# Performance work log

Measured on AMD Instinct MI355X. Metric: run time of the kernel, lower is better.

Reference implementation:

```python
import math
import jax, jax.numpy as jnp
import numpy as np
from jax import lax

B, S, ENC_IN = 8, 1024, 3
D_MODEL, N_HEADS, D_FF, E_LAYERS = 512, 8, 2048, 3
FACTOR, NUM_CLASS = 5, 5
EPS = 1e-5


def _positional_embedding(seq_len, d_model):
    pos = np.arange(seq_len)[:, None].astype(np.float32)
    div = np.exp(np.arange(0, d_model, 2).astype(np.float32) * -(math.log(10000.0) / d_model))
    pe = np.zeros((seq_len, d_model), dtype=np.float32)
    pe[:, 0::2] = np.sin(pos * div)
    pe[:, 1::2] = np.cos(pos * div)
    return jnp.asarray(pe)


def _layer_norm(x, g, b):
    mu = x.mean(-1, keepdims=True)
    var = ((x - mu) ** 2).mean(-1, keepdims=True)
    return (x - mu) / jnp.sqrt(var + EPS) * g + b


def _prob_attention(Q, K, V, key):
    # Q, K, V: (B, H, L, Dh). Informer ProbSparse self-attention (mask_flag=False).
    Bq, H, L, Dh = Q.shape
    sample_k = min(FACTOR * math.ceil(math.log(L)), L)  # U_part
    n_top = min(FACTOR * math.ceil(math.log(L)), L)     # u
    idx = jax.random.randint(key, (L, sample_k), 0, L)  # sampled key idx per query
    K_sample = K[:, :, idx, :]                          # (B,H,L,sample_k,Dh)
    QK_sample = jnp.einsum('bhld,bhlsd->bhls', Q, K_sample)
    M = QK_sample.max(-1) - QK_sample.sum(-1) / L       # sparsity measure (B,H,L)
    M_top = lax.top_k(M, n_top)[1]                      # (B,H,n_top)
    Q_reduce = jnp.take_along_axis(Q, M_top[..., None], axis=2)  # (B,H,n_top,Dh)
    scores = jnp.einsum('bhud,bhkd->bhuk', Q_reduce, K) / math.sqrt(Dh)
    attn = jax.nn.softmax(scores, axis=-1)
    upd = jnp.einsum('bhuk,bhkd->bhud', attn, V)        # (B,H,n_top,Dh)
    # initial context = mean of V over keys; active queries get real attention
    context = jnp.broadcast_to(V.mean(axis=2, keepdims=True), Q.shape)
    b_idx = jnp.arange(Bq)[:, None, None]
    h_idx = jnp.arange(H)[None, :, None]
    return context.at[b_idx, h_idx, M_top].set(upd)     # (B,H,L,Dh)


def _encoder_layer(x, p, key):
    (wq, bq, wk, bk, wv, bv, wo, bo, c1w, c1b, c2w, c2b, g1, b1, g2, b2) = p
    Bx, L, D = x.shape
    Dh = D // N_HEADS

    def heads(w, b_):
        return (x @ w.T + b_).reshape(Bx, L, N_HEADS, Dh).transpose(0, 2, 1, 3)

    Q, K, V = heads(wq, bq), heads(wk, bk), heads(wv, bv)
    ctx = _prob_attention(Q, K, V, key)
    new_x = ctx.transpose(0, 2, 1, 3).reshape(Bx, L, D) @ wo.T + bo
    x = _layer_norm(x + new_x, g1, b1)
    y = jax.nn.gelu(x @ c1w.T + c1b, approximate=False)  # 1x1 conv == matmul
    y = y @ c2w.T + c2b
    return _layer_norm(x + y, g2, b2)


def _forward(x_enc, x_mark_enc, token_kernel, Wq, bq, Wk, bk, Wv, bv, Wo, bo,
             c1w, c1b, c2w, c2b, g1, b1, g2, b2, gf, bf, proj_w, proj_b):
    # TokenEmbedding: circular Conv1d(enc_in -> d_model, kernel 3), no bias
    xp = jnp.concatenate([x_enc[:, -1:], x_enc, x_enc[:, :1]], axis=1)
    val = lax.conv_general_dilated(xp, token_kernel, (1,), 'VALID',
                                   dimension_numbers=('NWC', 'WIO', 'NWC'))
    x = val + _positional_embedding(S, D_MODEL)[None]  # dropout = 0 (eval)
    base = jax.random.key(42)
    for i in range(E_LAYERS):
        p = (Wq[i], bq[i], Wk[i], bk[i], Wv[i], bv[i], Wo[i], bo[i],
             c1w[i], c1b[i], c2w[i], c2b[i], g1[i], b1[i], g2[i], b2[i])
        x = _encoder_layer(x, p, jax.random.fold_in(base, i))
    x = _layer_norm(x, gf, bf)
    out = jax.nn.gelu(x, approximate=False)
    out = out * x_mark_enc[..., None]
    out = out.reshape(out.shape[0], -1)
    return out @ proj_w.T + proj_b  # (B, NUM_CLASS)


def setup_inputs():
    key = jax.random.key(0)
    ks = jax.random.split(key, 16)
    s = 0.02
    L, D, F = E_LAYERS, D_MODEL, D_FF

    def rn(k, shape, scale=s):
        return jax.random.normal(k, shape, jnp.float32) * scale

    return {
        'x_enc': jax.random.normal(ks[0], (B, S, ENC_IN), jnp.float32),
        'x_mark_enc': jnp.ones((B, S), jnp.float32),
        'token_kernel': rn(ks[1], (3, ENC_IN, D)),
        'Wq': rn(ks[2], (L, D, D)), 'bq': jnp.zeros((L, D), jnp.float32),
        'Wk': rn(ks[3], (L, D, D)), 'bk': jnp.zeros((L, D), jnp.float32),
        'Wv': rn(ks[4], (L, D, D)), 'bv': jnp.zeros((L, D), jnp.float32),
        'Wo': rn(ks[5], (L, D, D)), 'bo': jnp.zeros((L, D), jnp.float32),
        'c1w': rn(ks[6], (L, F, D)), 'c1b': jnp.zeros((L, F), jnp.float32),
        'c2w': rn(ks[7], (L, D, F)), 'c2b': jnp.zeros((L, D), jnp.float32),
        'g1': jnp.ones((L, D), jnp.float32), 'b1': jnp.zeros((L, D), jnp.float32),
        'g2': jnp.ones((L, D), jnp.float32), 'b2': jnp.zeros((L, D), jnp.float32),
        'gf': jnp.ones((D,), jnp.float32), 'bf': jnp.zeros((D,), jnp.float32),
        'proj_w': rn(ks[8], (NUM_CLASS, D * S), 0.002),
        'proj_b': jnp.zeros((NUM_CLASS,), jnp.float32),
    }


def reference(x_enc, x_mark_enc, token_kernel, Wq, bq, Wk, bk, Wv, bv, Wo, bo,
              c1w, c1b, c2w, c2b, g1, b1, g2, b2, gf, bf, proj_w, proj_b):
    return _forward(x_enc, x_mark_enc, token_kernel, Wq, bq, Wk, bk, Wv, bv, Wo, bo,
                    c1w, c1b, c2w, c2b, g1, b1, g2, b2, gf, bf, proj_w, proj_b)
```

## Files before the change

### kernel.cpp

```cpp
#include <hip/hip_runtime.h>
#include <hip/hip_bf16.h>
#include <stdint.h>


#define SQ 1024
#define DM 512
#define NH 8
#define DH 64
#define DFF 2048
#define NTOP 35
#define ROWS 8192
#define QKVD 1536
#define EPSF 1e-5f
#define KSPLIT 8
#define SSPLIT 4

typedef __attribute__((ext_vector_type(8))) short bf16x8;
typedef __attribute__((ext_vector_type(4))) float f32x4;

__device__ __forceinline__ void gload_lds16(const void* g, void* l) {
    __builtin_amdgcn_global_load_lds((const __attribute__((address_space(1))) void*)g,
                                     (__attribute__((address_space(3))) void*)l, 16, 0, 0);
}

__device__ inline float gelu_f(float v) {
    return 0.5f * v * (1.0f + erff(v * 0.7071067811865476f));
}

__device__ __forceinline__ void split_hl(float v, __hip_bfloat16& h, __hip_bfloat16& l) {
    h = __float2bfloat16(v);
    l = __float2bfloat16(v - __bfloat162float(h));
}

__device__ inline void tf_round(uint32_t& x0, uint32_t& x1, int r) {
    x0 += x1;
    x1 = (x1 << r) | (x1 >> (32 - r));
    x1 ^= x0;
}
__device__ inline uint2 tf2x32(uint32_t k0, uint32_t k1, uint32_t x0, uint32_t x1) {
    uint32_t ks2 = k0 ^ k1 ^ 0x1BD11BDAu;
    x0 += k0; x1 += k1;
    tf_round(x0,x1,13); tf_round(x0,x1,15); tf_round(x0,x1,26); tf_round(x0,x1,6);
    x0 += k1; x1 += ks2 + 1u;
    tf_round(x0,x1,17); tf_round(x0,x1,29); tf_round(x0,x1,16); tf_round(x0,x1,24);
    x0 += ks2; x1 += k0 + 2u;
    tf_round(x0,x1,13); tf_round(x0,x1,15); tf_round(x0,x1,26); tf_round(x0,x1,6);
    x0 += k0; x1 += k1 + 3u;
    tf_round(x0,x1,17); tf_round(x0,x1,29); tf_round(x0,x1,16); tf_round(x0,x1,24);
    x0 += k1; x1 += ks2 + 4u;
    tf_round(x0,x1,13); tf_round(x0,x1,15); tf_round(x0,x1,26); tf_round(x0,x1,6);
    x0 += ks2; x1 += k0 + 5u;
    return make_uint2(x0, x1);
}

__global__ void idx_kernel(int lyr, int* __restrict__ idx) {
    int p = blockIdx.x * 256 + threadIdx.x;
    if (p >= SQ * NTOP) return;
    uint2 fk = tf2x32(0u, 42u, 0u, (uint32_t)lyr);
    uint2 a = tf2x32(fk.x, fk.y, 0u, 2u);
    uint2 bb = tf2x32(fk.x, fk.y, 1u, 3u);
    uint32_t k20 = a.y, k21 = bb.y;
    const int half = (SQ * NTOP) / 2;
    uint32_t bits;
    if (p < half) bits = tf2x32(k20, k21, (uint32_t)p, (uint32_t)(half + p)).x;
    else          bits = tf2x32(k20, k21, (uint32_t)(p - half), (uint32_t)p).y;
    idx[p] = (int)(bits & 1023u);
}

__global__ __launch_bounds__(256) void embed_kernel(const float* __restrict__ xe,
                                                    const float* __restrict__ tk,
                                                    float* __restrict__ X,
                                                    __hip_bfloat16* __restrict__ Xh,
                                                    __hip_bfloat16* __restrict__ Xl) {
    int row = blockIdx.x;
    int b = row >> 10, s = row & 1023;
    __shared__ float xv[9];
    int t = threadIdx.x;
    if (t < 9) {
        int w = t / 3, c = t % 3;
        int tt = s + w;
        int r = (tt == 0) ? 1023 : (tt <= 1024 ? tt - 1 : 0);
        xv[t] = xe[((size_t)b * SQ + r) * 3 + c];
    }
    __syncthreads();
    const float cdiv = 0.017988946039015984f;
    for (int d = t; d < DM; d += 256) {
        float acc = 0.f;
        #pragma unroll
        for (int wi = 0; wi < 9; ++wi) acc += xv[wi] * tk[wi * DM + d];
        int j2 = (d >> 1) * 2;
        float div = expf(-cdiv * (float)j2);
        float ang = (float)s * div;
        float pe = (d & 1) ? cosf(ang) : sinf(ang);
        float v = acc + pe;
        size_t o = (size_t)row * DM + d;
        X[o] = v;
        __hip_bfloat16 hb, lb; split_hl(v, hb, lb);
        Xh[o] = hb; Xl[o] = lb;
    }
}

__global__ __launch_bounds__(256) void wsplitA_kernel(
    const float* __restrict__ Wq, const float* __restrict__ Wk,
    const float* __restrict__ Wv, const float* __restrict__ Wo,
    const float* __restrict__ bq, const float* __restrict__ bk,
    const float* __restrict__ bv,
    __hip_bfloat16* __restrict__ ha, __hip_bfloat16* __restrict__ la,
    __hip_bfloat16* __restrict__ hb, __hip_bfloat16* __restrict__ lb,
    float* __restrict__ biasC) {
    int t = threadIdx.x;
    if (blockIdx.x == 1024) {
        #pragma unroll
        for (int r = 0; r < 6; ++r) {
            int i = r * 256 + t;
            biasC[i] = (i < 512) ? bq[i] : (i < 1024) ? bk[i - 512] : bv[i - 1024];
        }
        return;
    }
    int i = blockIdx.x * 256 + t;
    int seg = i >> 16, local = i & 65535;
    const float* srcs[4] = {Wq, Wk, Wv, Wo};
    float4 v = reinterpret_cast<const float4*>(srcs[seg])[local];
    float vv[4] = {v.x, v.y, v.z, v.w};
    ushort hv[4], lv[4];
    #pragma unroll
    for (int j = 0; j < 4; ++j) {
        __hip_bfloat16 h_, l_; split_hl(vv[j], h_, l_);
        hv[j] = *reinterpret_cast<ushort*>(&h_);
        lv[j] = *reinterpret_cast<ushort*>(&l_);
    }
    ushort4 hq = make_ushort4(hv[0], hv[1], hv[2], hv[3]);
    ushort4 lq = make_ushort4(lv[0], lv[1], lv[2], lv[3]);
    if (seg < 3) {
        reinterpret_cast<ushort4*>(ha)[i] = hq;
        reinterpret_cast<ushort4*>(la)[i] = lq;
    } else {
        reinterpret_cast<ushort4*>(hb)[local] = hq;
        reinterpret_cast<ushort4*>(lb)[local] = lq;
    }
}

__global__ __launch_bounds__(256) void wsplitB_kernel(
    const float* __restrict__ c1w, const float* __restrict__ c2w,
    __hip_bfloat16* __restrict__ ha, __hip_bfloat16* __restrict__ la,
    __hip_bfloat16* __restrict__ hb, __hip_bfloat16* __restrict__ lb) {
    int i = blockIdx.x * 256 + threadIdx.x;
    int seg = i >> 18, local = i & 262143;
    const float* src = seg ? c2w : c1w;
    float4 v = reinterpret_cast<const float4*>(src)[local];
    float vv[4] = {v.x, v.y, v.z, v.w};
    ushort hv[4], lv[4];
    #pragma unroll
    for (int j = 0; j < 4; ++j) {
        __hip_bfloat16 h_, l_; split_hl(vv[j], h_, l_);
        hv[j] = *reinterpret_cast<ushort*>(&h_);
        lv[j] = *reinterpret_cast<ushort*>(&l_);
    }
    ushort4 hq = make_ushort4(hv[0], hv[1], hv[2], hv[3]);
    ushort4 lq = make_ushort4(lv[0], lv[1], lv[2], lv[3]);
    if (seg == 0) {
        reinterpret_cast<ushort4*>(ha)[local] = hq;
        reinterpret_cast<ushort4*>(la)[local] = lq;
    } else {
        reinterpret_cast<ushort4*>(hb)[local] = hq;
        reinterpret_cast<ushort4*>(lb)[local] = lq;
    }
}

template<int BN_, int OUTMODE, int NTERM>
__global__ __launch_bounds__(256) void mfma_gemm(
    const __hip_bfloat16* __restrict__ Ah, const __hip_bfloat16* __restrict__ Al,
    const __hip_bfloat16* __restrict__ Wh, const __hip_bfloat16* __restrict__ Wl,
    const float* __restrict__ bias,
    float* __restrict__ C,
    __hip_bfloat16* __restrict__ Oh, __hip_bfloat16* __restrict__ Ol,
    int M, int N, int K) {
    constexpr int NI = BN_ / 32;
    __shared__ __hip_bfloat16 As[128 * 64];
    __shared__ __hip_bfloat16 Bs[BN_ * 64];
    const int t = threadIdx.x;
    const int lane = t & 63, w = t >> 6;
    const int wm = w >> 1, wn = w & 1;
    const int bm = blockIdx.x * 128, bn = blockIdx.y * BN_;
    const int r15 = lane & 15, kc = lane >> 4;
    f32x4 acc[4][NI];
    #pragma unroll
    for (int mi = 0; mi < 4; ++mi)
        #pragma unroll
        for (int ni = 0; ni < NI; ++ni)
            acc[mi][ni] = (f32x4){0.f, 0.f, 0.f, 0.f};

    const int KT = NTERM * K;
    for (int kp = 0; kp < KT; kp += 64) {
        int seg = (NTERM == 3) ? ((kp >= 2 * K) ? 2 : ((kp >= K) ? 1 : 0))
                               : ((kp >= K) ? 1 : 0);
        int k0 = kp - seg * K;
        const __hip_bfloat16* Ab = (seg == 1) ? Al : Ah;
        const __hip_bfloat16* Bb = (NTERM == 3 && seg == 2) ? Wl : Wh;
        #pragma unroll
        for (int i = 0; i < 4; ++i) {
            int slot = i * 256 + t;
            int row = slot >> 3, cp = slot & 7;
            int cl = cp ^ (row & 7);
            gload_lds16(Ab + (size_t)(bm + row) * K + k0 + cl * 8, As + slot * 8);
        }
        #pragma unroll
        for (int i = 0; i < BN_ / 32; ++i) {
            int slot = i * 256 + t;
            int row = slot >> 3, cp = slot & 7;
            int cl = cp ^ (row & 7);
            gload_lds16(Bb + (size_t)(bn + row) * K + k0 + cl * 8, Bs + slot * 8);
        }
        __syncthreads();
        #pragma unroll
        for (int kk = 0; kk < 2; ++kk) {
            bf16x8 a[4], b[NI];
            #pragma unroll
            for (int mi = 0; mi < 4; ++mi) {
                int row = wm * 64 + mi * 16 + r15;
                int sl = ((kk << 2) | kc) ^ (row & 7);
                a[mi] = *reinterpret_cast<const bf16x8*>(As + row * 64 + sl * 8);
            }
            #pragma unroll
            for (int ni = 0; ni < NI; ++ni) {
                int row = wn * (BN_ / 2) + ni * 16 + r15;
                int sl = ((kk << 2) | kc) ^ (row & 7);
                b[ni] = *reinterpret_cast<const bf16x8*>(Bs + row * 64 + sl * 8);
            }
            #pragma unroll
            for (int mi = 0; mi < 4; ++mi)
                #pragma unroll
                for (int ni = 0; ni < NI; ++ni)
                    acc[mi][ni] = __builtin_amdgcn_mfma_f32_16x16x32_bf16(a[mi], b[ni], acc[mi][ni], 0, 0, 0);
        }
        __syncthreads();
    }

    const int rq = lane >> 4;
    #pragma unroll
    for (int mi = 0; mi < 4; ++mi) {
        #pragma unroll
        for (int ni = 0; ni < NI; ++ni) {
            int n = bn + wn * (BN_ / 2) + ni * 16 + r15;
            float bz = bias[n];
            #pragma unroll
            for (int r = 0; r < 4; ++r) {
                int m = bm + wm * 64 + mi * 16 + rq * 4 + r;
                float v = acc[mi][ni][r] + bz;
                if constexpr (OUTMODE == 0) {
                    C[(size_t)m * N + n] = v;
                } else {
                    float g = gelu_f(v);
                    __hip_bfloat16 hb, lb; split_hl(g, hb, lb);
                    Oh[(size_t)m * N + n] = hb;
                    Ol[(size_t)m * N + n] = lb;
                }
            }
        }
    }
}

__global__ __launch_bounds__(128) void mscore_part(const float* __restrict__ QKV,
                                                   const int* __restrict__ idx,
                                                   float* __restrict__ MX,
                                                   float* __restrict__ SM) {
    int bh = blockIdx.x;
    int l = blockIdx.y * 128 + threadIdx.x;
    int sc = blockIdx.z;
    int b = bh >> 3, h = bh & 7;
    const float4* q = reinterpret_cast<const float4*>(QKV + ((size_t)(b * SQ + l)) * QKVD + h * DH);
    float4 qr[16];
    #pragma unroll
    for (int i = 0; i < 16; ++i) qr[i] = q[i];
    int s0 = sc * 9;
    int s1 = (s0 + 9 < NTOP) ? s0 + 9 : NTOP;
    float mx = -INFINITY, sm = 0.f;
    for (int s = s0; s < s1; ++s) {
        int ki = idx[l * NTOP + s];
        const float4* kr = reinterpret_cast<const float4*>(QKV + ((size_t)(b * SQ + ki)) * QKVD + DM + h * DH);
        float d = 0.f;
        #pragma unroll
        for (int i = 0; i < 16; ++i) {
            float4 kv = kr[i];
            d += qr[i].x * kv.x + qr[i].y * kv.y + qr[i].z * kv.z + qr[i].w * kv.w;
        }
        mx = fmaxf(mx, d);
        sm += d;
    }
    size_t o = ((size_t)(bh * SSPLIT + sc) << 10) + l;
    MX[o] = mx; SM[o] = sm;
}

__global__ __launch_bounds__(256) void topk_kernel(const float* __restrict__ MX,
                                                   const float* __restrict__ SM,
                                                   int* __restrict__ Mtop) {
    int bh = blockIdx.x;
    int t = threadIdx.x, w = t >> 6, lane = t & 63;
    float v[4];
    #pragma unroll
    for (int j = 0; j < 4; ++j) {
        int i = j * 256 + t;
        float mx = -INFINITY, sm = 0.f;
        #pragma unroll
        for (int sc = 0; sc < SSPLIT; ++sc) {
            size_t o = ((size_t)(bh * SSPLIT + sc) << 10) + i;
            mx = fmaxf(mx, MX[o]);
            sm += SM[o];
        }
        v[j] = mx - sm * (1.0f / (float)SQ);
    }
    __shared__ float swv[4];
    __shared__ int swi[4];
    __shared__ int winner;
    for (int u = 0; u < NTOP; ++u) {
        float bv = v[0]; int bj = 0;
        #pragma unroll
        for (int j = 1; j < 4; ++j)
            if (v[j] > bv) { bv = v[j]; bj = j; }
        int bi = bj * 256 + t;
        #pragma unroll
        for (int off = 32; off; off >>= 1) {
            float ov = __shfl_xor(bv, off);
            int oi = __shfl_xor(bi, off);
            if (ov > bv || (ov == bv && oi < bi)) { bv = ov; bi = oi; }
        }
        if (lane == 0) { swv[w] = bv; swi[w] = bi; }
        __syncthreads();
        if (t == 0) {
            float gv = swv[0]; int gi = swi[0];
            #pragma unroll
            for (int k = 1; k < 4; ++k)
                if (swv[k] > gv || (swv[k] == gv && swi[k] < gi)) { gv = swv[k]; gi = swi[k]; }
            Mtop[bh * NTOP + u] = gi;
            winner = gi;
        }
        __syncthreads();
        int wi = winner;
        if ((wi & 255) == t) v[wi >> 8] = -INFINITY;
    }
}

__global__ __launch_bounds__(512) void attn_part(const float* __restrict__ QKV,
                                                 const int* __restrict__ Mtop,
                                                 float* __restrict__ PACC,
                                                 float* __restrict__ PM,
                                                 float* __restrict__ PL) {
    __shared__ float Qs[NTOP][68];
    __shared__ float Kt[64][68];
    __shared__ float Vt[64][68];
    __shared__ float St[NTOP][64];
    __shared__ float mS[NTOP], lS[NTOP], fS[NTOP];
    __shared__ int qidx[NTOP];
    int bh = blockIdx.x, ks = blockIdx.y;
    int b = bh >> 3, h = bh & 7;
    int t = threadIdx.x, w = t >> 6, lane = t & 63;
    if (t < NTOP) { qidx[t] = Mtop[bh * NTOP + t]; mS[t] = -INFINITY; lS[t] = 0.f; }
    __syncthreads();
    for (int u = w; u < NTOP; u += 8)
        Qs[u][lane] = QKV[((size_t)(b * SQ + qidx[u])) * QKVD + h * DH + lane];
    float a_acc[5] = {0.f, 0.f, 0.f, 0.f, 0.f};
    __syncthreads();
    for (int tk = ks * 2; tk < ks * 2 + 2; ++tk) {
        #pragma unroll
        for (int i = 0; i < 2; ++i) {
            int idx4 = i * 512 + t;
            int kr = idx4 >> 4, c4 = (idx4 & 15) << 2;
            const float* kp = QKV + ((size_t)(b * SQ + tk * 64 + kr)) * QKVD + DM + h * DH + c4;
            *reinterpret_cast<float4*>(&Kt[kr][c4]) = *reinterpret_cast<const float4*>(kp);
            *reinterpret_cast<float4*>(&Vt[kr][c4]) = *reinterpret_cast<const float4*>(kp + DM);
        }
        __syncthreads();
        float sv[5] = {0.f, 0.f, 0.f, 0.f, 0.f};
        #pragma unroll
        for (int d4 = 0; d4 < 16; ++d4) {
            float4 kv = *reinterpret_cast<const float4*>(&Kt[lane][d4 << 2]);
            #pragma unroll
            for (int j = 0; j < 5; ++j) {
                int u = w + 8 * j;
                if (u < NTOP) {
                    float4 qv = *reinterpret_cast<const float4*>(&Qs[u][d4 << 2]);
                    sv[j] += qv.x * kv.x + qv.y * kv.y + qv.z * kv.z + qv.w * kv.w;
                }
            }
        }
        #pragma unroll
        for (int j = 0; j < 5; ++j) {
            int u = w + 8 * j;
            if (u < NTOP) {
                float s = sv[j] * 0.125f;
                float mx = s;
                #pragma unroll
                for (int off = 32; off; off >>= 1) mx = fmaxf(mx, __shfl_xor(mx, off));
                float m_old = mS[u];
                float m_new = fmaxf(m_old, mx);
                float e = expf(s - m_new);
                float sum = e;
                #pragma unroll
                for (int off = 32; off; off >>= 1) sum += __shfl_xor(sum, off);
                St[u][lane] = e;
                if (lane == 0) {
                    float f = expf(m_old - m_new);
                    fS[u] = f;
                    lS[u] = lS[u] * f + sum;
                    mS[u] = m_new;
                }
            }
        }
        __syncthreads();
        #pragma unroll
        for (int j = 0; j < 5; ++j) {
            int u = w + 8 * j;
            if (u < NTOP) {
                float acc = a_acc[j] * fS[u];
                for (int k = 0; k < 64; ++k)
                    acc += St[u][k] * Vt[k][lane];
                a_acc[j] = acc;
            }
        }
        __syncthreads();
    }
    #pragma unroll
    for (int j = 0; j < 5; ++j) {
        int u = w + 8 * j;
        if (u < NTOP) {
            PACC[(((size_t)bh * KSPLIT + ks) * NTOP + u) * DH + lane] = a_acc[j];
            if (lane == 0) {
                PM[((size_t)bh * KSPLIT + ks) * NTOP + u] = mS[u];
                PL[((size_t)bh * KSPLIT + ks) * NTOP + u] = lS[u];
            }
        }
    }
}

__global__ __launch_bounds__(512) void attn_comb(const float* __restrict__ PACC,
                                                 const float* __restrict__ PM,
                                                 const float* __restrict__ PL,
                                                 const int* __restrict__ Mtop,
                                                 __hip_bfloat16* __restrict__ ch,
                                                 __hip_bfloat16* __restrict__ cl) {
    int bh = blockIdx.x;
    int b = bh >> 3, h = bh & 7;
    int t = threadIdx.x, w = t >> 6, lane = t & 63;
    #pragma unroll
    for (int j = 0; j < 5; ++j) {
        int u = w + 8 * j;
        if (u < NTOP) {
            float M = -INFINITY;
            #pragma unroll
            for (int i = 0; i < KSPLIT; ++i)
                M = fmaxf(M, PM[((size_t)bh * KSPLIT + i) * NTOP + u]);
            float lsum = 0.f, acc = 0.f;
            #pragma unroll
            for (int i = 0; i < KSPLIT; ++i) {
                float f = expf(PM[((size_t)bh * KSPLIT + i) * NTOP + u] - M);
                lsum += f * PL[((size_t)bh * KSPLIT + i) * NTOP + u];
                acc += f * PACC[(((size_t)bh * KSPLIT + i) * NTOP + u) * DH + lane];
            }
            float v = acc / lsum;
            int l = Mtop[bh * NTOP + u];
            size_t o = ((size_t)(b * SQ + l)) * DM + h * DH + lane;
            __hip_bfloat16 hb, lb; split_hl(v, hb, lb);
            ch[o] = hb; cl[o] = lb;
        }
    }
}

__global__ __launch_bounds__(256) void meanv_part(const float* __restrict__ QKV,
                                                  float* __restrict__ part) {
    int bh = blockIdx.x, sp = blockIdx.y;
    int t = threadIdx.x;
    int b = bh >> 3, h = bh & 7;
    int dh = t & 63, chunk = t >> 6;
    int s0 = sp * 128 + chunk * 32;
    float acc = 0.f;
    for (int s = s0; s < s0 + 32; ++s)
        acc += QKV[((size_t)(b * SQ + s)) * QKVD + 2 * DM + h * DH + dh];
    __shared__ float red[256];
    red[t] = acc; __syncthreads();
    if (t < 64)
        part[((size_t)bh * 8 + sp) * DH + dh] =
            red[t] + red[64 + t] + red[128 + t] + red[192 + t];
}

__global__ void meanv_comb(const float* __restrict__ part, float* __restrict__ meanV) {
    int bh = blockIdx.x;
    int t = threadIdx.x;
    float s = 0.f;
    #pragma unroll
    for (int i = 0; i < 8; ++i) s += part[((size_t)bh * 8 + i) * DH + t];
    meanV[bh * DH + t] = s * (1.0f / (float)SQ);
}

__global__ void ctxfill2_kernel(const float* __restrict__ meanV,
                                __hip_bfloat16* __restrict__ ch,
                                __hip_bfloat16* __restrict__ cl) {
    int n = blockIdx.x * 256 + threadIdx.x;
    int d = n & 511;
    int row = n >> 9;
    int b = row >> 10;
    float v = meanV[((b << 3) + (d >> 6)) * DH + (d & 63)];
    __hip_bfloat16 hb, lb; split_hl(v, hb, lb);
    ch[n] = hb; cl[n] = lb;
}

__global__ __launch_bounds__(256) void add_ln_kernel(const float* __restrict__ Av,
                                                     const float* __restrict__ Bv,
                                                     const float* __restrict__ g,
                                                     const float* __restrict__ be,
                                                     float* __restrict__ out,
                                                     __hip_bfloat16* __restrict__ oh,
                                                     __hip_bfloat16* __restrict__ ol) {
    int row = blockIdx.x;
    int t = threadIdx.x;
    size_t base = (size_t)row * DM;
    float v0 = Av[base + t] + Bv[base + t];
    float v1 = Av[base + 256 + t] + Bv[base + 256 + t];
    __shared__ float r1[256], r2[256];
    r1[t] = v0 + v1; r2[t] = v0 * v0 + v1 * v1;
    __syncthreads();
    for (int s = 128; s > 0; s >>= 1) {
        if (t < s) { r1[t] += r1[t + s]; r2[t] += r2[t + s]; }
        __syncthreads();
    }
    float mu = r1[0] * (1.0f / (float)DM);
    float var = r2[0] * (1.0f / (float)DM) - mu * mu;
    float rs = rsqrtf(var + EPSF);
    float o0 = (v0 - mu) * rs * g[t] + be[t];
    float o1 = (v1 - mu) * rs * g[t + 256] + be[t + 256];
    out[base + t] = o0;
    out[base + 256 + t] = o1;
    __hip_bfloat16 hb, lb;
    split_hl(o0, hb, lb); oh[base + t] = hb; ol[base + t] = lb;
    split_hl(o1, hb, lb); oh[base + 256 + t] = hb; ol[base + 256 + t] = lb;
}

__global__ __launch_bounds__(256) void final_kernel(const float* __restrict__ X,
                                                    const float* __restrict__ g,
                                                    const float* __restrict__ be,
                                                    const float* __restrict__ mark,
                                                    float* __restrict__ act) {
    int row = blockIdx.x;
    int t = threadIdx.x;
    size_t base = (size_t)row * DM;
    float v0 = X[base + t];
    float v1 = X[base + 256 + t];
    __shared__ float r1[256], r2[256];
    r1[t] = v0 + v1; r2[t] = v0 * v0 + v1 * v1;
    __syncthreads();
    for (int s = 128; s > 0; s >>= 1) {
        if (t < s) { r1[t] += r1[t + s]; r2[t] += r2[t + s]; }
        __syncthreads();
    }
    float mu = r1[0] * (1.0f / (float)DM);
    float var = r2[0] * (1.0f / (float)DM) - mu * mu;
    float rs = rsqrtf(var + EPSF);
    float mk = mark[row];
    float a0 = (v0 - mu) * rs * g[t] + be[t];
    float a1 = (v1 - mu) * rs * g[t + 256] + be[t + 256];
    act[base + t] = gelu_f(a0) * mk;
    act[base + 256 + t] = gelu_f(a1) * mk;
}

__global__ __launch_bounds__(256) void proj1_kernel(const float* __restrict__ act,
                                                    const float* __restrict__ pw,
                                                    float* __restrict__ part) {
    int bc = blockIdx.x;
    int sg = blockIdx.y;
    int b = bc / 5, c = bc % 5;
    const float4* a = reinterpret_cast<const float4*>(act + (size_t)b * (SQ * DM) + sg * 32768);
    const float4* w = reinterpret_cast<const float4*>(pw + (size_t)c * (SQ * DM) + sg * 32768);
    float s = 0.f;
    for (int i = threadIdx.x; i < 8192; i += 256) {
        float4 av = a[i], wv = w[i];
        s += av.x * wv.x + av.y * wv.y + av.z * wv.z + av.w * wv.w;
    }
    __shared__ float red[256];
    red[threadIdx.x] = s; __syncthreads();
    for (int sft = 128; sft > 0; sft >>= 1) {
        if (threadIdx.x < sft) red[threadIdx.x] += red[threadIdx.x + sft];
        __syncthreads();
    }
    if (threadIdx.x == 0) part[bc * 16 + sg] = red[0];
}

__global__ void proj2_kernel(const float* __restrict__ part, const float* __restrict__ pb,
                             float* __restrict__ out) {
    int t = threadIdx.x;
    if (t < 40) {
        float s = 0.f;
        #pragma unroll
        for (int i = 0; i < 16; ++i) s += part[t * 16 + i];
        out[t] = s + pb[t % 5];
    }
}

extern "C" void kernel_launch(void* const* d_in, const int* in_sizes, int n_in,
                              void* d_out, int out_size, void* d_ws, size_t ws_size,
                              hipStream_t stream) {
    (void)in_sizes; (void)n_in; (void)out_size; (void)ws_size;

    const float* x_enc      = (const float*)d_in[0];
    const float* x_mark_enc = (const float*)d_in[1];
    const float* token_k    = (const float*)d_in[2];
    const float* Wq = (const float*)d_in[3];
    const float* bq = (const float*)d_in[4];
    const float* Wk = (const float*)d_in[5];
    const float* bk = (const float*)d_in[6];
    const float* Wv = (const float*)d_in[7];
    const float* bv = (const float*)d_in[8];
    const float* Wo = (const float*)d_in[9];
    const float* bo = (const float*)d_in[10];
    const float* c1w = (const float*)d_in[11];
    const float* c1b = (const float*)d_in[12];
    const float* c2w = (const float*)d_in[13];
    const float* c2b = (const float*)d_in[14];
    const float* g1 = (const float*)d_in[15];
    const float* b1 = (const float*)d_in[16];
    const float* g2 = (const float*)d_in[17];
    const float* b2 = (const float*)d_in[18];
    const float* gf = (const float*)d_in[19];
    const float* bf = (const float*)d_in[20];
    const float* proj_w = (const float*)d_in[21];
    const float* proj_b = (const float*)d_in[22];
    float* out = (float*)d_out;

    const size_t MB = 1024 * 1024;
    char* wsb = (char*)d_ws;
    float* X    = (float*)(wsb);
    float* QKVp = (float*)(wsb + 16 * MB);
    __hip_bfloat16* CTXh = (__hip_bfloat16*)(wsb + 16 * MB);
    __hip_bfloat16* CTXl = (__hip_bfloat16*)(wsb + 24 * MB);
    __hip_bfloat16* Yh   = (__hip_bfloat16*)(wsb);
    __hip_bfloat16* Yl   = (__hip_bfloat16*)(wsb + 32 * MB);
    float* X1p  = (float*)(wsb + 64 * MB);
    float* NXp  = (float*)(wsb + 80 * MB);
    __hip_bfloat16* Xh  = (__hip_bfloat16*)(wsb + 96 * MB);
    __hip_bfloat16* Xl  = (__hip_bfloat16*)(wsb + 104 * MB);
    __hip_bfloat16* X1h = (__hip_bfloat16*)(wsb + 112 * MB);
    __hip_bfloat16* X1l = (__hip_bfloat16*)(wsb + 120 * MB);
    __hip_bfloat16* WhA = (__hip_bfloat16*)(wsb + 128 * MB);
    __hip_bfloat16* WlA = (__hip_bfloat16*)(wsb + 130 * MB);
    __hip_bfloat16* WhB = (__hip_bfloat16*)(wsb + 132 * MB);
    __hip_bfloat16* WlB = (__hip_bfloat16*)(wsb + 134 * MB);
    char* smal = wsb + 136 * MB;
    float* biasC  = (float*)(smal);
    int*   IDX    = (int*)(smal + 8 * 1024);
    int*   MTOP   = (int*)(smal + 168 * 1024);
    float* MEANV  = (float*)(smal + 184 * 1024);
    float* PART   = (float*)(smal + 200 * 1024);
    float* MVPART = (float*)(smal + 208 * 1024);
    float* MX     = (float*)(smal + 384 * 1024);
    float* SM     = (float*)(smal + 2176 * 1024);
    float* PM     = (float*)(smal + 3968 * 1024);
    float* PL     = (float*)(smal + 4064 * 1024);
    float* PACC   = (float*)(smal + 4160 * 1024);

    embed_kernel<<<ROWS, 256, 0, stream>>>(x_enc, token_k, X, Xh, Xl);

    for (int lyr = 0; lyr < 3; ++lyr) {
        const float* Wq_l = Wq + (size_t)lyr * DM * DM;
        const float* bq_l = bq + (size_t)lyr * DM;
        const float* Wk_l = Wk + (size_t)lyr * DM * DM;
        const float* bk_l = bk + (size_t)lyr * DM;
        const float* Wv_l = Wv + (size_t)lyr * DM * DM;
        const float* bv_l = bv + (size_t)lyr * DM;
        const float* Wo_l = Wo + (size_t)lyr * DM * DM;
        const float* bo_l = bo + (size_t)lyr * DM;
        const float* c1w_l = c1w + (size_t)lyr * DFF * DM;
        const float* c1b_l = c1b + (size_t)lyr * DFF;
        const float* c2w_l = c2w + (size_t)lyr * DM * DFF;
        const float* c2b_l = c2b + (size_t)lyr * DM;
        const float* g1_l = g1 + (size_t)lyr * DM;
        const float* b1_l = b1 + (size_t)lyr * DM;
        const float* g2_l = g2 + (size_t)lyr * DM;
        const float* b2_l = b2 + (size_t)lyr * DM;

        wsplitA_kernel<<<1025, 256, 0, stream>>>(Wq_l, Wk_l, Wv_l, Wo_l,
                                                 bq_l, bk_l, bv_l,
                                                 WhA, WlA, WhB, WlB, biasC);
        mfma_gemm<128, 0, 3><<<dim3(ROWS / 128, QKVD / 128), 256, 0, stream>>>(
            Xh, Xl, WhA, WlA, biasC, QKVp, nullptr, nullptr, ROWS, QKVD, DM);

        idx_kernel<<<(SQ * NTOP + 255) / 256, 256, 0, stream>>>(lyr, IDX);
        mscore_part<<<dim3(64, 8, SSPLIT), 128, 0, stream>>>(QKVp, IDX, MX, SM);
        topk_kernel<<<64, 256, 0, stream>>>(MX, SM, MTOP);
        attn_part<<<dim3(64, KSPLIT), 512, 0, stream>>>(QKVp, MTOP, PACC, PM, PL);
        meanv_part<<<dim3(64, 8), 256, 0, stream>>>(QKVp, MVPART);
        meanv_comb<<<64, 64, 0, stream>>>(MVPART, MEANV);
        ctxfill2_kernel<<<(ROWS * DM) / 256, 256, 0, stream>>>(MEANV, CTXh, CTXl);
        attn_comb<<<64, 512, 0, stream>>>(PACC, PM, PL, MTOP, CTXh, CTXl);

        mfma_gemm<64, 0, 2><<<dim3(ROWS / 128, DM / 64), 256, 0, stream>>>(
            CTXh, CTXl, WhB, WlB, bo_l, NXp, nullptr, nullptr, ROWS, DM, DM);
        add_ln_kernel<<<ROWS, 256, 0, stream>>>(X, NXp, g1_l, b1_l, X1p, X1h, X1l);

        wsplitB_kernel<<<2048, 256, 0, stream>>>(c1w_l, c2w_l, WhA, WlA, WhB, WlB);
        mfma_gemm<128, 2, 2><<<dim3(ROWS / 128, DFF / 128), 256, 0, stream>>>(
            X1h, X1l, WhA, WlA, c1b_l, nullptr, Yh, Yl, ROWS, DFF, DM);
        mfma_gemm<64, 0, 2><<<dim3(ROWS / 128, DM / 64), 256, 0, stream>>>(
            Yh, Yl, WhB, WlB, c2b_l, NXp, nullptr, nullptr, ROWS, DM, DFF);
        add_ln_kernel<<<ROWS, 256, 0, stream>>>(X1p, NXp, g2_l, b2_l, X, Xh, Xl);
    }

    final_kernel<<<ROWS, 256, 0, stream>>>(X, gf, bf, x_mark_enc, (float*)QKVp);
    proj1_kernel<<<dim3(40, 16), 256, 0, stream>>>((float*)QKVp, proj_w, PART);
    proj2_kernel<<<1, 64, 0, stream>>>(PART, proj_b, out);
}
```

Before: 1.373 ms.

## Compute sparsity scores with 16 lanes per query and shuffle reduction

The sparsity-measure kernel now assigns each query row to 16 lanes, each holding one float4 of Q. Each sampled K row is read as a coalesced 256-byte access and the dot product is reduced with xor shuffles. This replaces one thread per query reading a full K row, which produced scattered per-thread loads, plus the 4-way split across sample chunks. The split partials are gone, so topk reads the final max and sum directly. The cost is four shuffle rounds per sampled key and more threads in total.

```diff
diff --git a/kernel.cpp b/kernel.cpp
--- a/kernel.cpp
+++ b/kernel.cpp
@@ -13,7 +13,6 @@
 #define QKVD 1536
 #define EPSF 1e-5f
 #define KSPLIT 8
-#define SSPLIT 4
 
 typedef __attribute__((ext_vector_type(8))) short bf16x8;
 typedef __attribute__((ext_vector_type(4))) float f32x4;
@@ -260,35 +259,36 @@
     }
 }
 
-__global__ __launch_bounds__(128) void mscore_part(const float* __restrict__ QKV,
+__global__ __launch_bounds__(512) void mscore_wave(const float* __restrict__ QKV,
                                                    const int* __restrict__ idx,
                                                    float* __restrict__ MX,
                                                    float* __restrict__ SM) {
     int bh = blockIdx.x;
-    int l = blockIdx.y * 128 + threadIdx.x;
-    int sc = blockIdx.z;
     int b = bh >> 3, h = bh & 7;
-    const float4* q = reinterpret_cast<const float4*>(QKV + ((size_t)(b * SQ + l)) * QKVD + h * DH);
-    float4 qr[16];
-    #pragma unroll
-    for (int i = 0; i < 16; ++i) qr[i] = q[i];
-    int s0 = sc * 9;
-    int s1 = (s0 + 9 < NTOP) ? s0 + 9 : NTOP;
+    int t = threadIdx.x;
+    int wv = t >> 6, lane = t & 63;
+    int r = lane >> 4;
+    int d4 = lane & 15;
+    int l = blockIdx.y * 32 + wv * 4 + r;
+    const float* qbase = QKV + ((size_t)(b * SQ + l)) * QKVD + h * DH;
+    float4 q = reinterpret_cast<const float4*>(qbase)[d4];
+    const float* Kbase = QKV + (size_t)b * SQ * QKVD + DM + h * DH;
+    const int* ib = idx + l * NTOP;
     float mx = -INFINITY, sm = 0.f;
-    for (int s = s0; s < s1; ++s) {
-        int ki = idx[l * NTOP + s];
-        const float4* kr = reinterpret_cast<const float4*>(QKV + ((size_t)(b * SQ + ki)) * QKVD + DM + h * DH);
-        float d = 0.f;
-        #pragma unroll
-        for (int i = 0; i < 16; ++i) {
-            float4 kv = kr[i];
-            d += qr[i].x * kv.x + qr[i].y * kv.y + qr[i].z * kv.z + qr[i].w * kv.w;
-        }
+    #pragma unroll 7
+    for (int s = 0; s < NTOP; ++s) {
+        int ki = ib[s];
+        float4 kv = reinterpret_cast<const float4*>(Kbase + (size_t)ki * QKVD)[d4];
+        float d = q.x * kv.x + q.y * kv.y + q.z * kv.z + q.w * kv.w;
+        #pragma unroll
+        for (int off = 8; off; off >>= 1) d += __shfl_xor(d, off);
         mx = fmaxf(mx, d);
         sm += d;
     }
-    size_t o = ((size_t)(bh * SSPLIT + sc) << 10) + l;
-    MX[o] = mx; SM[o] = sm;
+    if (d4 == 0) {
+        MX[bh * SQ + l] = mx;
+        SM[bh * SQ + l] = sm;
+    }
 }
 
 __global__ __launch_bounds__(256) void topk_kernel(const float* __restrict__ MX,
@@ -300,14 +300,8 @@
     #pragma unroll
     for (int j = 0; j < 4; ++j) {
         int i = j * 256 + t;
-        float mx = -INFINITY, sm = 0.f;
-        #pragma unroll
-        for (int sc = 0; sc < SSPLIT; ++sc) {
-            size_t o = ((size_t)(bh * SSPLIT + sc) << 10) + i;
-            mx = fmaxf(mx, MX[o]);
-            sm += SM[o];
-        }
-        v[j] = mx - sm * (1.0f / (float)SQ);
+        size_t o = (size_t)bh * SQ + i;
+        v[j] = MX[o] - SM[o] * (1.0f / (float)SQ);
     }
     __shared__ float swv[4];
     __shared__ int swi[4];
@@ -682,7 +676,7 @@
             Xh, Xl, WhA, WlA, biasC, QKVp, nullptr, nullptr, ROWS, QKVD, DM);
 
         idx_kernel<<<(SQ * NTOP + 255) / 256, 256, 0, stream>>>(lyr, IDX);
-        mscore_part<<<dim3(64, 8, SSPLIT), 128, 0, stream>>>(QKVp, IDX, MX, SM);
+        mscore_wave<<<dim3(64, 32), 512, 0, stream>>>(QKVp, IDX, MX, SM);
         topk_kernel<<<64, 256, 0, stream>>>(MX, SM, MTOP);
         attn_part<<<dim3(64, KSPLIT), 512, 0, stream>>>(QKVp, MTOP, PACC, PM, PL);
         meanv_part<<<dim3(64, 8), 256, 0, stream>>>(QKVp, MVPART);
```

After: 1.201 ms. 1.14x faster.
